# Performance work log

Measured on AMD Instinct MI355X. Metric: run time of the kernel, lower is better.

## Reference

```python
import jax, jax.numpy as jnp
import numpy as np

B, C, H, W = 2, 128, 64, 64


def setup_inputs() -> dict:
    key = jax.random.key(0)
    ks = jax.random.split(key, 16)
    s = 1.0 / np.sqrt(C)
    d = {
        "x": jax.random.normal(ks[0], (B, C, H, W), jnp.float32),
        "y": jax.random.normal(ks[1], (B, C, H, W), jnp.float32),
    }
    names = ["qr", "qi", "kr", "ki", "vr", "vi"]
    for i, n in enumerate(names):
        d["W" + n] = jax.random.normal(ks[2 + 2 * i], (C, C), jnp.float32) * s
        d["b" + n] = jax.random.normal(ks[3 + 2 * i], (C,), jnp.float32) * s
    return d


def _lin(t, Wt, bt):
    # t: [b, n, c]; torch Linear: t @ W^T + b
    return jnp.einsum("bnc,dc->bnd", t, Wt) + bt


def reference(x, y, Wqr, bqr, Wqi, bqi, Wkr, bkr, Wki, bki, Wvr, bvr, Wvi, bvi):
    b, c, h, w = x.shape
    xf = jnp.fft.fft2(x)  # over last two axes (h, w)
    yf = jnp.fft.fft2(y)
    # b c h w -> b (h w) c
    def flat(t):
        return t.transpose(0, 2, 3, 1).reshape(b, h * w, c)
    xr, xi = flat(xf.real), flat(xf.imag)
    yr, yi = flat(yf.real), flat(yf.imag)

    Qr = _lin(xr, Wqr, bqr) - _lin(xi, Wqi, bqi)
    Qi = _lin(xi, Wqr, bqr) + _lin(xr, Wqi, bqi)
    Kr = _lin(yr, Wkr, bkr) - _lin(yi, Wki, bki)
    Ki = _lin(yi, Wkr, bkr) + _lin(yr, Wki, bki)
    Vr = _lin(yr, Wvr, bvr) - _lin(yi, Wvi, bvi)
    Vi = _lin(yi, Wvr, bvr) + _lin(yr, Wvi, bvi)

    sr = jnp.einsum("bnc,bmc->bnm", Qr, Kr) - jnp.einsum("bnc,bmc->bnm", Qi, Ki)
    si = jnp.einsum("bnc,bmc->bnm", Qr, Ki) + jnp.einsum("bnc,bmc->bnm", Qi, Kr)
    scores = jnp.sqrt(sr * sr + si * si + 1e-8)
    attn = jax.nn.softmax(scores, axis=-1)

    out_r = jnp.einsum("bnm,bmc->bnc", attn, Vr)
    out_i = jnp.einsum("bnm,bmc->bnc", attn, Vi)
    out_c = jax.lax.complex(out_r, out_i)
    # b (h w) c -> b c h w
    out_c = out_c.reshape(b, h, w, c).transpose(0, 3, 1, 2)
    return jnp.fft.ifft2(out_c).real
```

## Files before the change

kernel.cpp:

```cpp
#include <hip/hip_runtime.h>
#include <math.h>


#define PI2 6.283185307179586f

typedef __attribute__((ext_vector_type(8))) short short8;
typedef __attribute__((ext_vector_type(4))) float f32x4;

#define MFMA16(A,B,C) __builtin_amdgcn_mfma_f32_16x16x32_bf16((A),(B),(C),0,0,0)

__device__ inline unsigned short f2bf(float x){
  union{float f; unsigned int u;} a; a.f = x;
  unsigned int r = (a.u + 0x7fffu + ((a.u>>16)&1u)) >> 16;
  return (unsigned short)r;
}
__device__ inline float bf2f(unsigned short h){
  union{unsigned int u; float f;} a; a.u = ((unsigned int)h)<<16; return a.f;
}
__device__ inline short8 neg8(short8 x){
  union{short8 v; unsigned int u[4];} a; a.v = x;
  a.u[0]^=0x80008000u; a.u[1]^=0x80008000u; a.u[2]^=0x80008000u; a.u[3]^=0x80008000u;
  return a.v;
}
__device__ inline void gload_lds16(const void* g, void* lds){
  __builtin_amdgcn_global_load_lds((const __attribute__((address_space(1))) unsigned int*)g,
                                   (__attribute__((address_space(3))) unsigned int*)lds,
                                   16, 0, 0);
}

__global__ __launch_bounds__(256) void dft2_fwd_kernel(
    const float* __restrict__ x, const float* __restrict__ y,
    float* __restrict__ xr, float* __restrict__ xi,
    float* __restrict__ yr, float* __restrict__ yi)
{
  __shared__ float Xs[4096];
  __shared__ float Tr[4096], Ti[4096];
  __shared__ float twc[64], tws[64];
  int blk = blockIdx.x;
  const float* src; float *outr, *outi;
  int plane;
  if (blk < 256) { src = x; outr = xr; outi = xi; plane = blk; }
  else           { src = y; outr = yr; outi = yi; plane = blk - 256; }
  int b = plane >> 7, c = plane & 127;
  int t = threadIdx.x;
  if (t < 64) {
    float ang = -PI2 * (float)t / 64.0f;
    twc[t] = cosf(ang); tws[t] = sinf(ang);
  }
  const float* p = src + ((size_t)plane << 12);
  for (int i = t; i < 4096; i += 256) Xs[i] = p[i];
  __syncthreads();
  for (int j = 0; j < 16; j++) {
    int o = t + 256 * j; int h = o >> 6, wp = o & 63;
    float ar = 0.f, ai = 0.f;
    for (int w = 0; w < 64; w++) {
      int k = (w * wp) & 63;
      float v = Xs[h * 64 + w];
      ar = fmaf(v, twc[k], ar);
      ai = fmaf(v, tws[k], ai);
    }
    Tr[h * 64 + wp] = ar; Ti[h * 64 + wp] = ai;
  }
  __syncthreads();
  size_t ob = ((size_t)b * 4096) * 128 + c;
  for (int j = 0; j < 16; j++) {
    int o = t + 256 * j; int hp = o >> 6, wp = o & 63;
    float ar = 0.f, ai = 0.f;
    for (int h = 0; h < 64; h++) {
      int k = (h * hp) & 63;
      float cr = twc[k], ci = tws[k];
      float tr = Tr[h * 64 + wp], ti = Ti[h * 64 + wp];
      ar += tr * cr - ti * ci;
      ai += tr * ci + ti * cr;
    }
    int n = (hp << 6) + wp;
    outr[ob + (size_t)n * 128] = ar;
    outi[ob + (size_t)n * 128] = ai;
  }
}

__global__ __launch_bounds__(256) void proj_kernel(
    const float* __restrict__ xr, const float* __restrict__ xi,
    const float* __restrict__ yr, const float* __restrict__ yi,
    const float* __restrict__ Wqr, const float* __restrict__ bqr,
    const float* __restrict__ Wqi, const float* __restrict__ bqi,
    const float* __restrict__ Wkr, const float* __restrict__ bkr,
    const float* __restrict__ Wki, const float* __restrict__ bki,
    const float* __restrict__ Wvr, const float* __restrict__ bvr,
    const float* __restrict__ Wvi, const float* __restrict__ bvi,
    unsigned short* __restrict__ FQ, unsigned short* __restrict__ FK,
    unsigned short* __restrict__ FV)
{
  __shared__ float Asr[64 * 33], Asi[64 * 33], Wsr[128 * 33], Wsi[128 * 33];
  int nt = blockIdx.x, lin = blockIdx.y, b = blockIdx.z;
  const float *ar, *ai, *Wr, *Wi, *br_, *bi_;
  unsigned short* F;
  if (lin == 0)      { ar = xr; ai = xi; Wr = Wqr; Wi = Wqi; br_ = bqr; bi_ = bqi; F = FQ; }
  else if (lin == 1) { ar = yr; ai = yi; Wr = Wkr; Wi = Wki; br_ = bkr; bi_ = bki; F = FK; }
  else               { ar = yr; ai = yi; Wr = Wvr; Wi = Wvi; br_ = bvr; bi_ = bvi; F = FV; }
  int t = threadIdx.x; int td = t & 15, tn = t >> 4;
  int n0 = nt * 64;
  size_t abase = (size_t)b * 4096 * 128 + (size_t)n0 * 128;
  const size_t PS = (size_t)2 * 4096 * 128;
  float accr[4][8] = {}, acci[4][8] = {};
  for (int kk = 0; kk < 4; kk++) {
    __syncthreads();
    for (int idx = t; idx < 64 * 32; idx += 256) {
      int r = idx >> 5, ccol = idx & 31;
      Asr[r * 33 + ccol] = ar[abase + (size_t)r * 128 + kk * 32 + ccol];
      Asi[r * 33 + ccol] = ai[abase + (size_t)r * 128 + kk * 32 + ccol];
    }
    for (int idx = t; idx < 128 * 32; idx += 256) {
      int r = idx >> 5, ccol = idx & 31;
      Wsr[r * 33 + ccol] = Wr[(size_t)r * 128 + kk * 32 + ccol];
      Wsi[r * 33 + ccol] = Wi[(size_t)r * 128 + kk * 32 + ccol];
    }
    __syncthreads();
    for (int k = 0; k < 32; k++) {
      float a_r[4], a_i[4], w_r[8], w_i[8];
      #pragma unroll
      for (int i = 0; i < 4; i++) {
        a_r[i] = Asr[(tn * 4 + i) * 33 + k];
        a_i[i] = Asi[(tn * 4 + i) * 33 + k];
      }
      #pragma unroll
      for (int jj = 0; jj < 8; jj++) {
        w_r[jj] = Wsr[(td + 16 * jj) * 33 + k];
        w_i[jj] = Wsi[(td + 16 * jj) * 33 + k];
      }
      #pragma unroll
      for (int i = 0; i < 4; i++)
        #pragma unroll
        for (int jj = 0; jj < 8; jj++) {
          accr[i][jj] += a_r[i] * w_r[jj] - a_i[i] * w_i[jj];
          acci[i][jj] += a_i[i] * w_r[jj] + a_r[i] * w_i[jj];
        }
    }
  }
  for (int jj = 0; jj < 8; jj++) {
    int d = td + 16 * jj;
    float brd = br_[d], bid = bi_[d];
    #pragma unroll
    for (int i = 0; i < 4; i++) {
      int n = n0 + tn * 4 + i;
      float cr = accr[i][jj] + (brd - bid);
      float ci = acci[i][jj] + (brd + bid);
      size_t base = ((size_t)b * 4096 + n) * 128 + d;
      if (lin <= 1) {
        unsigned short rh = f2bf(cr); unsigned short rl = f2bf(cr - bf2f(rh));
        unsigned short ih = f2bf(ci); unsigned short il = f2bf(ci - bf2f(ih));
        F[0 * PS + base] = rh;
        F[1 * PS + base] = rl;
        F[2 * PS + base] = ih;
        F[3 * PS + base] = il;
      } else {
        F[0 * PS + base] = f2bf(cr);
        F[1 * PS + base] = f2bf(ci);
      }
    }
  }
}

__global__ __launch_bounds__(256) void kpack_kernel(
    const unsigned short* __restrict__ F, unsigned short* __restrict__ Kpk)
{
  int blk = blockIdx.x;
  int b = blk >> 6, mt = blk & 63;
  int t = threadIdx.x;
  size_t obase = (size_t)blk * 4096;
  #pragma unroll
  for (int k = 0; k < 16; k++) {
    int idx = t + 256 * k;
    int l = idx & 63, s = (idx >> 6) & 3, tml = (idx >> 8) & 3, a = idx >> 10;
    int n = mt * 64 + tml * 16 + (l & 15);
    int c0 = 32 * s + 8 * (l >> 4);
    const short8 v = *(const short8*)(F + (((size_t)(a * 2 + b) * 4096 + n) * 128 + c0));
    *(short8*)(Kpk + (obase + idx) * 8) = v;
  }
}

__global__ __launch_bounds__(256) void vpack_kernel(
    const unsigned short* __restrict__ F, unsigned short* __restrict__ Vpk)
{
  __shared__ unsigned short Vs[2 * 32 * 128];
  int blk = blockIdx.x;
  int b = blk >> 7, sm = blk & 127;
  int t = threadIdx.x;
  const size_t PS = (size_t)2 * 4096 * 128;
  #pragma unroll
  for (int p = 0; p < 2; p++) {
    #pragma unroll
    for (int k = 0; k < 2; k++) {
      int idx8 = t + 256 * k;
      int nn = idx8 >> 4, d0 = (idx8 & 15) * 8;
      const short8 v = *(const short8*)(F + p * PS + ((size_t)(b * 4096 + sm * 32 + nn)) * 128 + d0);
      *(short8*)(Vs + (p * 32 + nn) * 128 + d0) = v;
    }
  }
  __syncthreads();
  size_t obase = (size_t)blk * 1024;
  #pragma unroll
  for (int k = 0; k < 4; k++) {
    int idx = t + 256 * k;
    int lv = idx & 63, tc = idx >> 6;
    int vh = tc >> 3;
    int d = (tc & 7) * 16 + (lv & 15);
    int nb = (lv >> 4) * 8;
    short8 v;
    #pragma unroll
    for (int j = 0; j < 8; j++)
      v[j] = (short)Vs[(vh * 32 + nb + j) * 128 + d];
    *(short8*)(Vpk + (obase + idx) * 8) = v;
  }
}

__global__ __launch_bounds__(256, 2) void attn_mfma_kernel(
    const unsigned short* __restrict__ FQ, const short* __restrict__ Kpk,
    const short* __restrict__ Vpk,
    float* __restrict__ Or_, float* __restrict__ Oi_)
{
  __shared__ __align__(16) short Klds[32768];
  __shared__ __align__(16) short Pfrag[16 * 72];
  __shared__ __align__(16) float rmax[16][4];

  const int bi = blockIdx.x;
  const int xg = bi & 7;
  const int b = xg >> 2;
  const int qt2 = (bi >> 3) * 4 + (xg & 3);
  const int t = threadIdx.x;
  const int ms = t >> 6, l = t & 63;
  const int g = l >> 4, c = l & 15;

  const size_t PS = (size_t)2 * 4096 * 128;
  short8 Qf[4][4];
  #pragma unroll
  for (int a = 0; a < 4; a++)
    #pragma unroll
    for (int s = 0; s < 4; s++)
      Qf[a][s] = *(const short8*)(FQ + (size_t)a * PS +
                 ((size_t)(b * 4096) + qt2 * 16 + c) * 128 + 32 * s + 8 * g);

  f32x4 O[4], Oe;
  #pragma unroll
  for (int nt = 0; nt < 4; nt++) O[nt] = (f32x4){0.f, 0.f, 0.f, 0.f};
  Oe = (f32x4){0.f, 0.f, 0.f, 0.f};
  float Mq = -3e38f, escPrev = 1.0f;
  bool upPrev = false;
  short8 Vreg[2][4];
  const short b1 = (short)0x3F80;
  const short8 ones = {b1, b1, b1, b1, b1, b1, b1, b1};
  const short8* Vp8 = (const short8*)Vpk;

  auto STAGE = [&](int tile) {
    const char* gsrc = (const char*)Kpk + ((size_t)(b * 64 + tile) << 16);
    #pragma unroll
    for (int i2 = 0; i2 < 16; i2++) {
      int ch = ms * 16 + i2;
      gload_lds16(gsrc + ch * 1024 + l * 16, (char*)Klds + ch * 1024);
    }
  };

  STAGE(0);
  asm volatile("s_waitcnt vmcnt(0)" ::: "memory");
  __builtin_amdgcn_s_barrier();
  __builtin_amdgcn_sched_barrier(0);

  f32x4 s0;
  for (int mt = 0; mt < 64; mt++) {
    if (mt > 0) {
      if (upPrev) {
        f32x4 esc4;
        #pragma unroll
        for (int r = 0; r < 4; r++) esc4[r] = __shfl(escPrev, 4 * g + r);
        #pragma unroll
        for (int r = 0; r < 4; r++) {
          #pragma unroll
          for (int nt = 0; nt < 4; nt++) O[nt][r] *= esc4[r];
          Oe[r] *= esc4[r];
        }
      }
      __builtin_amdgcn_s_setprio(1);
      #pragma unroll
      for (int ks = 0; ks < 2; ks++) {
        short8 Pa = *(const short8*)&Pfrag[c * 72 + 32 * ks + 8 * g];
        #pragma unroll
        for (int nt = 0; nt < 4; nt++)
          O[nt] = MFMA16(Pa, Vreg[ks][nt], O[nt]);
        Oe = MFMA16(Pa, ones, Oe);
      }
      __builtin_amdgcn_s_setprio(0);
    }
    const short8* kb8 = (const short8*)Klds;
    f32x4 sr0 = (f32x4){0,0,0,0}, sr1 = (f32x4){0,0,0,0};
    f32x4 si0 = (f32x4){0,0,0,0}, si1 = (f32x4){0,0,0,0};
    __builtin_amdgcn_s_setprio(1);
    #pragma unroll
    for (int s = 0; s < 4; s++) {
      short8 Arh = kb8[((0 * 4 + ms) * 4 + s) * 64 + l];
      short8 Arl = kb8[((1 * 4 + ms) * 4 + s) * 64 + l];
      short8 Aih = kb8[((2 * 4 + ms) * 4 + s) * 64 + l];
      short8 Ail = kb8[((3 * 4 + ms) * 4 + s) * 64 + l];
      short8 nqh = neg8(Qf[2][s]);
      short8 nql = neg8(Qf[3][s]);
      f32x4& sr = (s & 1) ? sr1 : sr0;
      f32x4& si = (s & 1) ? si1 : si0;
      sr = MFMA16(Arh, Qf[0][s], sr);
      si = MFMA16(Arh, Qf[2][s], si);
      sr = MFMA16(Arh, Qf[1][s], sr);
      si = MFMA16(Arh, Qf[3][s], si);
      sr = MFMA16(Arl, Qf[0][s], sr);
      si = MFMA16(Arl, Qf[2][s], si);
      sr = MFMA16(Aih, nqh, sr);
      si = MFMA16(Aih, Qf[0][s], si);
      sr = MFMA16(Aih, nql, sr);
      si = MFMA16(Aih, Qf[1][s], si);
      sr = MFMA16(Ail, nqh, sr);
      si = MFMA16(Ail, Qf[0][s], si);
    }
    __builtin_amdgcn_s_setprio(0);
    #pragma unroll
    for (int r = 0; r < 4; r++) {
      float a2 = sr0[r] + sr1[r], b2 = si0[r] + si1[r];
      s0[r] = sqrtf(a2 * a2 + b2 * b2 + 1e-8f);
    }
    float mloc = fmaxf(fmaxf(s0[0], s0[1]), fmaxf(s0[2], s0[3]));
    mloc = fmaxf(mloc, __shfl_xor(mloc, 16));
    mloc = fmaxf(mloc, __shfl_xor(mloc, 32));
    if (l < 16) rmax[l][ms] = mloc;
    asm volatile("s_waitcnt lgkmcnt(0)" ::: "memory");
    __builtin_amdgcn_s_barrier();
    __builtin_amdgcn_sched_barrier(0);
    if (mt + 1 < 64) STAGE(mt + 1);
    {
      f32x4 rm4 = *(const f32x4*)&rmax[c][0];
      float cand = fmaxf(fmaxf(rm4[0], rm4[1]), fmaxf(rm4[2], rm4[3]));
      bool up = !__all((int)(cand <= Mq + 8.0f));
      if (up) {
        float Mnew = fmaxf(Mq, cand);
        escPrev = __expf(Mq - Mnew);
        Mq = Mnew;
      }
      upPrev = up;
      f32x4 p;
      #pragma unroll
      for (int r = 0; r < 4; r++) p[r] = __expf(s0[r] - Mq);
      unsigned int* pw = (unsigned int*)&Pfrag[c * 72 + 16 * ms + 4 * g];
      pw[0] = (unsigned int)f2bf(p[0]) | ((unsigned int)f2bf(p[1]) << 16);
      pw[1] = (unsigned int)f2bf(p[2]) | ((unsigned int)f2bf(p[3]) << 16);
      #pragma unroll
      for (int ks = 0; ks < 2; ks++)
        #pragma unroll
        for (int nt = 0; nt < 4; nt++)
          Vreg[ks][nt] = Vp8[((size_t)((b * 128 + mt * 2 + ks) * 16 + ms * 4 + nt)) * 64 + l];
    }
    __builtin_amdgcn_sched_barrier(0);
    asm volatile("s_waitcnt vmcnt(8) lgkmcnt(0)" ::: "memory");
    __builtin_amdgcn_s_barrier();
    __builtin_amdgcn_sched_barrier(0);
  }
  {
    if (upPrev) {
      f32x4 esc4;
      #pragma unroll
      for (int r = 0; r < 4; r++) esc4[r] = __shfl(escPrev, 4 * g + r);
      #pragma unroll
      for (int r = 0; r < 4; r++) {
        #pragma unroll
        for (int nt = 0; nt < 4; nt++) O[nt][r] *= esc4[r];
        Oe[r] *= esc4[r];
      }
    }
    #pragma unroll
    for (int ks = 0; ks < 2; ks++) {
      short8 Pa = *(const short8*)&Pfrag[c * 72 + 32 * ks + 8 * g];
      #pragma unroll
      for (int nt = 0; nt < 4; nt++)
        O[nt] = MFMA16(Pa, Vreg[ks][nt], O[nt]);
      Oe = MFMA16(Pa, ones, Oe);
    }
  }
  const size_t base = (size_t)b * 4096 * 128;
  f32x4 inv;
  #pragma unroll
  for (int r = 0; r < 4; r++) inv[r] = 1.0f / Oe[r];
  #pragma unroll
  for (int nt = 0; nt < 4; nt++) {
    int cc = ms * 64 + nt * 16 + c;
    #pragma unroll
    for (int r = 0; r < 4; r++) {
      int row = qt2 * 16 + 4 * g + r;
      float v = O[nt][r] * inv[r];
      if (cc < 128) Or_[base + (size_t)row * 128 + cc] = v;
      else          Oi_[base + (size_t)row * 128 + cc - 128] = v;
    }
  }
}

__global__ __launch_bounds__(256) void idft2_kernel(
    const float* __restrict__ Or_, const float* __restrict__ Oi_,
    float* __restrict__ out)
{
  __shared__ float Ar[4096], Ai[4096], Tr[4096], Ti[4096];
  __shared__ float twc[64], tws[64];
  int plane = blockIdx.x; int b = plane >> 7, c = plane & 127;
  int t = threadIdx.x;
  if (t < 64) {
    float ang = PI2 * (float)t / 64.0f;
    twc[t] = cosf(ang); tws[t] = sinf(ang);
  }
  size_t ibase = (size_t)b * 4096 * 128 + c;
  for (int i = t; i < 4096; i += 256) {
    Ar[i] = Or_[ibase + (size_t)i * 128];
    Ai[i] = Oi_[ibase + (size_t)i * 128];
  }
  __syncthreads();
  for (int j = 0; j < 16; j++) {
    int o = t + 256 * j; int hp = o >> 6, w = o & 63;
    float tr = 0.f, ti = 0.f;
    for (int wp = 0; wp < 64; wp++) {
      int k = (wp * w) & 63;
      float cr = twc[k], ci = tws[k];
      float ar = Ar[hp * 64 + wp], ai = Ai[hp * 64 + wp];
      tr += ar * cr - ai * ci;
      ti += ai * cr + ar * ci;
    }
    Tr[hp * 64 + w] = tr; Ti[hp * 64 + w] = ti;
  }
  __syncthreads();
  size_t obase = ((size_t)plane) << 12;
  for (int j = 0; j < 16; j++) {
    int o = t + 256 * j; int h = o >> 6, w = o & 63;
    float acc = 0.f;
    for (int hp = 0; hp < 64; hp++) {
      int k = (hp * h) & 63;
      acc += Tr[hp * 64 + w] * twc[k] - Ti[hp * 64 + w] * tws[k];
    }
    out[obase + o] = acc * (1.0f / 4096.0f);
  }
}

extern "C" void kernel_launch(void* const* d_in, const int* in_sizes, int n_in,
                              void* d_out, int out_size, void* d_ws, size_t ws_size,
                              hipStream_t stream) {
  const float* x   = (const float*)d_in[0];
  const float* y   = (const float*)d_in[1];
  const float* Wqr = (const float*)d_in[2];  const float* bqr = (const float*)d_in[3];
  const float* Wqi = (const float*)d_in[4];  const float* bqi = (const float*)d_in[5];
  const float* Wkr = (const float*)d_in[6];  const float* bkr = (const float*)d_in[7];
  const float* Wki = (const float*)d_in[8];  const float* bki = (const float*)d_in[9];
  const float* Wvr = (const float*)d_in[10]; const float* bvr = (const float*)d_in[11];
  const float* Wvi = (const float*)d_in[12]; const float* bvi = (const float*)d_in[13];
  char* wsb = (char*)d_ws;
  if (ws_size < ((size_t)40 << 20)) return;
  unsigned short* FQ  = (unsigned short*)(wsb);
  unsigned short* FK  = (unsigned short*)(wsb + ((size_t)8  << 20));
  unsigned short* FV  = (unsigned short*)(wsb + ((size_t)16 << 20));
  float* xr = (float*)(wsb + ((size_t)20 << 20));
  float* xi = (float*)(wsb + ((size_t)24 << 20));
  float* yr = (float*)(wsb + ((size_t)28 << 20));
  float* yi = (float*)(wsb + ((size_t)32 << 20));
  unsigned short* Kpk = (unsigned short*)(wsb + ((size_t)28 << 20));
  unsigned short* Vpk = (unsigned short*)(wsb + ((size_t)36 << 20));
  float* Or_ = (float*)(wsb + ((size_t)20 << 20));
  float* Oi_ = (float*)(wsb + ((size_t)24 << 20));
  float* out = (float*)d_out;

  hipLaunchKernelGGL(dft2_fwd_kernel, dim3(512), dim3(256), 0, stream,
                     x, y, xr, xi, yr, yi);
  hipLaunchKernelGGL(proj_kernel, dim3(64, 3, 2), dim3(256), 0, stream,
                     xr, xi, yr, yi,
                     Wqr, bqr, Wqi, bqi, Wkr, bkr, Wki, bki, Wvr, bvr, Wvi, bvi,
                     FQ, FK, FV);
  hipLaunchKernelGGL(kpack_kernel, dim3(128), dim3(256), 0, stream, FK, Kpk);
  hipLaunchKernelGGL(vpack_kernel, dim3(256), dim3(256), 0, stream, FV, Vpk);
  hipLaunchKernelGGL(attn_mfma_kernel, dim3(512), dim3(256), 0, stream,
                     FQ, (const short*)Kpk, (const short*)Vpk, Or_, Oi_);
  hipLaunchKernelGGL(idft2_kernel, dim3(256), dim3(256), 0, stream,
                     Or_, Oi_, out);
}
```

Before: 405.0 us.

## Prefetch K tile into registers and issue next-tile staging earlier

Each wave now reads its whole K tile from LDS into registers at the top of the loop. It then immediately starts the global-to-LDS staging of the next tile instead of waiting until after the softmax-max barrier. The staging chunk mapping is reordered so each wave overwrites only the LDS chunks it has just read, which avoids any cross-wave hazard. V register loads are also moved earlier so they overlap the QK MFMAs. The aim is more overlap of global memory latency with compute, at the cost of about 64 extra VGPRs per lane for the K registers, which may reduce occupancy.

```diff
diff --git a/kernel.cpp b/kernel.cpp
--- a/kernel.cpp
+++ b/kernel.cpp
@@ -254,10 +254,12 @@
   auto STAGE = [&](int tile) {
     const char* gsrc = (const char*)Kpk + ((size_t)(b * 64 + tile) << 16);
     #pragma unroll
-    for (int i2 = 0; i2 < 16; i2++) {
-      int ch = ms * 16 + i2;
-      gload_lds16(gsrc + ch * 1024 + l * 16, (char*)Klds + ch * 1024);
-    }
+    for (int a = 0; a < 4; a++)
+      #pragma unroll
+      for (int s = 0; s < 4; s++) {
+        int ch = (a * 4 + ms) * 4 + s;
+        gload_lds16(gsrc + ch * 1024 + l * 16, (char*)Klds + ch * 1024);
+      }
   };
 
   STAGE(0);
@@ -265,8 +267,19 @@
   __builtin_amdgcn_s_barrier();
   __builtin_amdgcn_sched_barrier(0);
 
+  const short8* kb8 = (const short8*)Klds;
   f32x4 s0;
   for (int mt = 0; mt < 64; mt++) {
+    short8 Kreg[4][4];
+    #pragma unroll
+    for (int p = 0; p < 4; p++)
+      #pragma unroll
+      for (int s = 0; s < 4; s++)
+        Kreg[p][s] = kb8[((p * 4 + ms) * 4 + s) * 64 + l];
+    asm volatile("s_waitcnt lgkmcnt(0)" ::: "memory");
+    __builtin_amdgcn_sched_barrier(0);
+    if (mt + 1 < 64) STAGE(mt + 1);
+    __builtin_amdgcn_sched_barrier(0);
     if (mt > 0) {
       if (upPrev) {
         f32x4 esc4;
@@ -290,32 +303,33 @@
       }
       __builtin_amdgcn_s_setprio(0);
     }
-    const short8* kb8 = (const short8*)Klds;
+    #pragma unroll
+    for (int ks = 0; ks < 2; ks++)
+      #pragma unroll
+      for (int nt = 0; nt < 4; nt++)
+        Vreg[ks][nt] = Vp8[((size_t)((b * 128 + mt * 2 + ks) * 16 + ms * 4 + nt)) * 64 + l];
+    __builtin_amdgcn_sched_barrier(0);
     f32x4 sr0 = (f32x4){0,0,0,0}, sr1 = (f32x4){0,0,0,0};
     f32x4 si0 = (f32x4){0,0,0,0}, si1 = (f32x4){0,0,0,0};
     __builtin_amdgcn_s_setprio(1);
     #pragma unroll
     for (int s = 0; s < 4; s++) {
-      short8 Arh = kb8[((0 * 4 + ms) * 4 + s) * 64 + l];
-      short8 Arl = kb8[((1 * 4 + ms) * 4 + s) * 64 + l];
-      short8 Aih = kb8[((2 * 4 + ms) * 4 + s) * 64 + l];
-      short8 Ail = kb8[((3 * 4 + ms) * 4 + s) * 64 + l];
       short8 nqh = neg8(Qf[2][s]);
       short8 nql = neg8(Qf[3][s]);
       f32x4& sr = (s & 1) ? sr1 : sr0;
       f32x4& si = (s & 1) ? si1 : si0;
-      sr = MFMA16(Arh, Qf[0][s], sr);
-      si = MFMA16(Arh, Qf[2][s], si);
-      sr = MFMA16(Arh, Qf[1][s], sr);
-      si = MFMA16(Arh, Qf[3][s], si);
-      sr = MFMA16(Arl, Qf[0][s], sr);
-      si = MFMA16(Arl, Qf[2][s], si);
-      sr = MFMA16(Aih, nqh, sr);
-      si = MFMA16(Aih, Qf[0][s], si);
-      sr = MFMA16(Aih, nql, sr);
-      si = MFMA16(Aih, Qf[1][s], si);
-      sr = MFMA16(Ail, nqh, sr);
-      si = MFMA16(Ail, Qf[0][s], si);
+      sr = MFMA16(Kreg[0][s], Qf[0][s], sr);
+      si = MFMA16(Kreg[0][s], Qf[2][s], si);
+      sr = MFMA16(Kreg[0][s], Qf[1][s], sr);
+      si = MFMA16(Kreg[0][s], Qf[3][s], si);
+      sr = MFMA16(Kreg[1][s], Qf[0][s], sr);
+      si = MFMA16(Kreg[1][s], Qf[2][s], si);
+      sr = MFMA16(Kreg[2][s], nqh, sr);
+      si = MFMA16(Kreg[2][s], Qf[0][s], si);
+      sr = MFMA16(Kreg[2][s], nql, sr);
+      si = MFMA16(Kreg[2][s], Qf[1][s], si);
+      sr = MFMA16(Kreg[3][s], nqh, sr);
+      si = MFMA16(Kreg[3][s], Qf[0][s], si);
     }
     __builtin_amdgcn_s_setprio(0);
     #pragma unroll
@@ -330,7 +344,6 @@
     asm volatile("s_waitcnt lgkmcnt(0)" ::: "memory");
     __builtin_amdgcn_s_barrier();
     __builtin_amdgcn_sched_barrier(0);
-    if (mt + 1 < 64) STAGE(mt + 1);
     {
       f32x4 rm4 = *(const f32x4*)&rmax[c][0];
       float cand = fmaxf(fmaxf(rm4[0], rm4[1]), fmaxf(rm4[2], rm4[3]));
@@ -347,11 +360,6 @@
       unsigned int* pw = (unsigned int*)&Pfrag[c * 72 + 16 * ms + 4 * g];
       pw[0] = (unsigned int)f2bf(p[0]) | ((unsigned int)f2bf(p[1]) << 16);
       pw[1] = (unsigned int)f2bf(p[2]) | ((unsigned int)f2bf(p[3]) << 16);
-      #pragma unroll
-      for (int ks = 0; ks < 2; ks++)
-        #pragma unroll
-        for (int nt = 0; nt < 4; nt++)
-          Vreg[ks][nt] = Vp8[((size_t)((b * 128 + mt * 2 + ks) * 16 + ms * 4 + nt)) * 64 + l];
     }
     __builtin_amdgcn_sched_barrier(0);
     asm volatile("s_waitcnt vmcnt(8) lgkmcnt(0)" ::: "memory");
```

Measured after the change: 419.4 us. 1.04x slower.

## Software-pipeline attention loop to overlap QK of next tile with softmax/PV

Applied to the files above, without the earlier changes.

Restructures the attention main loop into a skewed pipeline: each iteration computes QK scores for tile mt while the softmax and PV for tile mt-1 (and PV for mt-2) run in the same iteration. Pfrag and rmax get double buffers indexed by parity, which removes one block barrier per iteration. The intent is to hide the barrier and softmax latency behind MFMA work. The cost is more live registers and a more complex prologue and epilogue. The STAGE load order is also reordered so chunks follow the (a,ms,s) indexing.

```diff
diff --git a/kernel.cpp b/kernel.cpp
--- a/kernel.cpp
+++ b/kernel.cpp
@@ -220,8 +220,8 @@
     float* __restrict__ Or_, float* __restrict__ Oi_)
 {
   __shared__ __align__(16) short Klds[32768];
-  __shared__ __align__(16) short Pfrag[16 * 72];
-  __shared__ __align__(16) float rmax[16][4];
+  __shared__ __align__(16) short Pfrag2[2][16 * 72];
+  __shared__ __align__(16) float rmax2[2][16][4];
 
   const int bi = blockIdx.x;
   const int xg = bi & 7;
@@ -250,47 +250,19 @@
   const short b1 = (short)0x3F80;
   const short8 ones = {b1, b1, b1, b1, b1, b1, b1, b1};
   const short8* Vp8 = (const short8*)Vpk;
+  const short8* kb8 = (const short8*)Klds;
 
   auto STAGE = [&](int tile) {
     const char* gsrc = (const char*)Kpk + ((size_t)(b * 64 + tile) << 16);
     #pragma unroll
-    for (int i2 = 0; i2 < 16; i2++) {
-      int ch = ms * 16 + i2;
-      gload_lds16(gsrc + ch * 1024 + l * 16, (char*)Klds + ch * 1024);
-    }
-  };
-
-  STAGE(0);
-  asm volatile("s_waitcnt vmcnt(0)" ::: "memory");
-  __builtin_amdgcn_s_barrier();
-  __builtin_amdgcn_sched_barrier(0);
-
-  f32x4 s0;
-  for (int mt = 0; mt < 64; mt++) {
-    if (mt > 0) {
-      if (upPrev) {
-        f32x4 esc4;
-        #pragma unroll
-        for (int r = 0; r < 4; r++) esc4[r] = __shfl(escPrev, 4 * g + r);
-        #pragma unroll
-        for (int r = 0; r < 4; r++) {
-          #pragma unroll
-          for (int nt = 0; nt < 4; nt++) O[nt][r] *= esc4[r];
-          Oe[r] *= esc4[r];
-        }
+    for (int a = 0; a < 4; a++)
+      #pragma unroll
+      for (int s = 0; s < 4; s++) {
+        int ch = (a * 4 + ms) * 4 + s;
+        gload_lds16(gsrc + ch * 1024 + l * 16, (char*)Klds + ch * 1024);
       }
-      __builtin_amdgcn_s_setprio(1);
-      #pragma unroll
-      for (int ks = 0; ks < 2; ks++) {
-        short8 Pa = *(const short8*)&Pfrag[c * 72 + 32 * ks + 8 * g];
-        #pragma unroll
-        for (int nt = 0; nt < 4; nt++)
-          O[nt] = MFMA16(Pa, Vreg[ks][nt], O[nt]);
-        Oe = MFMA16(Pa, ones, Oe);
-      }
-      __builtin_amdgcn_s_setprio(0);
-    }
-    const short8* kb8 = (const short8*)Klds;
+  };
+  auto QK = [&](f32x4& sout) {
     f32x4 sr0 = (f32x4){0,0,0,0}, sr1 = (f32x4){0,0,0,0};
     f32x4 si0 = (f32x4){0,0,0,0}, si1 = (f32x4){0,0,0,0};
     __builtin_amdgcn_s_setprio(1);
@@ -321,64 +293,111 @@
     #pragma unroll
     for (int r = 0; r < 4; r++) {
       float a2 = sr0[r] + sr1[r], b2 = si0[r] + si1[r];
-      s0[r] = sqrtf(a2 * a2 + b2 * b2 + 1e-8f);
-    }
+      sout[r] = sqrtf(a2 * a2 + b2 * b2 + 1e-8f);
+    }
+  };
+  auto WRMAX = [&](const f32x4& s0, int par) {
     float mloc = fmaxf(fmaxf(s0[0], s0[1]), fmaxf(s0[2], s0[3]));
     mloc = fmaxf(mloc, __shfl_xor(mloc, 16));
     mloc = fmaxf(mloc, __shfl_xor(mloc, 32));
-    if (l < 16) rmax[l][ms] = mloc;
+    if (l < 16) rmax2[par][l][ms] = mloc;
+  };
+  auto LOADV = [&](int mt) {
+    #pragma unroll
+    for (int ks = 0; ks < 2; ks++)
+      #pragma unroll
+      for (int nt = 0; nt < 4; nt++)
+        Vreg[ks][nt] = Vp8[((size_t)((b * 128 + mt * 2 + ks) * 16 + ms * 4 + nt)) * 64 + l];
+  };
+  auto RESCALE = [&]() {
+    f32x4 esc4;
+    #pragma unroll
+    for (int r = 0; r < 4; r++) esc4[r] = __shfl(escPrev, 4 * g + r);
+    #pragma unroll
+    for (int r = 0; r < 4; r++) {
+      #pragma unroll
+      for (int nt = 0; nt < 4; nt++) O[nt][r] *= esc4[r];
+      Oe[r] *= esc4[r];
+    }
+  };
+  auto PV = [&](int par) {
+    __builtin_amdgcn_s_setprio(1);
+    #pragma unroll
+    for (int ks = 0; ks < 2; ks++) {
+      short8 Pa = *(const short8*)&Pfrag2[par][c * 72 + 32 * ks + 8 * g];
+      #pragma unroll
+      for (int nt = 0; nt < 4; nt++)
+        O[nt] = MFMA16(Pa, Vreg[ks][nt], O[nt]);
+      Oe = MFMA16(Pa, ones, Oe);
+    }
+    __builtin_amdgcn_s_setprio(0);
+  };
+  auto SOFTMAX = [&](const f32x4& sPrev, int par) {
+    f32x4 rm4 = *(const f32x4*)&rmax2[par][c][0];
+    float cand = fmaxf(fmaxf(rm4[0], rm4[1]), fmaxf(rm4[2], rm4[3]));
+    bool up = !__all((int)(cand <= Mq + 8.0f));
+    if (up) {
+      float Mnew = fmaxf(Mq, cand);
+      escPrev = __expf(Mq - Mnew);
+      Mq = Mnew;
+    }
+    upPrev = up;
+    f32x4 p;
+    #pragma unroll
+    for (int r = 0; r < 4; r++) p[r] = __expf(sPrev[r] - Mq);
+    unsigned int* pw = (unsigned int*)&Pfrag2[par][c * 72 + 16 * ms + 4 * g];
+    pw[0] = (unsigned int)f2bf(p[0]) | ((unsigned int)f2bf(p[1]) << 16);
+    pw[1] = (unsigned int)f2bf(p[2]) | ((unsigned int)f2bf(p[3]) << 16);
+  };
+
+  STAGE(0);
+  asm volatile("s_waitcnt vmcnt(0)" ::: "memory");
+  __builtin_amdgcn_s_barrier();
+  __builtin_amdgcn_sched_barrier(0);
+
+  f32x4 s0prev, s0new;
+  QK(s0prev);
+  asm volatile("s_waitcnt lgkmcnt(0)" ::: "memory");
+  __builtin_amdgcn_sched_barrier(0);
+  STAGE(1);
+  __builtin_amdgcn_sched_barrier(0);
+  WRMAX(s0prev, 0);
+  asm volatile("s_waitcnt vmcnt(0) lgkmcnt(0)" ::: "memory");
+  __builtin_amdgcn_s_barrier();
+  __builtin_amdgcn_sched_barrier(0);
+
+  for (int mt = 1; mt < 64; mt++) {
+    const int p = mt & 1;
+    QK(s0new);
     asm volatile("s_waitcnt lgkmcnt(0)" ::: "memory");
-    __builtin_amdgcn_s_barrier();
     __builtin_amdgcn_sched_barrier(0);
     if (mt + 1 < 64) STAGE(mt + 1);
-    {
-      f32x4 rm4 = *(const f32x4*)&rmax[c][0];
-      float cand = fmaxf(fmaxf(rm4[0], rm4[1]), fmaxf(rm4[2], rm4[3]));
-      bool up = !__all((int)(cand <= Mq + 8.0f));
-      if (up) {
-        float Mnew = fmaxf(Mq, cand);
-        escPrev = __expf(Mq - Mnew);
-        Mq = Mnew;
-      }
-      upPrev = up;
-      f32x4 p;
-      #pragma unroll
-      for (int r = 0; r < 4; r++) p[r] = __expf(s0[r] - Mq);
-      unsigned int* pw = (unsigned int*)&Pfrag[c * 72 + 16 * ms + 4 * g];
-      pw[0] = (unsigned int)f2bf(p[0]) | ((unsigned int)f2bf(p[1]) << 16);
-      pw[1] = (unsigned int)f2bf(p[2]) | ((unsigned int)f2bf(p[3]) << 16);
-      #pragma unroll
-      for (int ks = 0; ks < 2; ks++)
-        #pragma unroll
-        for (int nt = 0; nt < 4; nt++)
-          Vreg[ks][nt] = Vp8[((size_t)((b * 128 + mt * 2 + ks) * 16 + ms * 4 + nt)) * 64 + l];
-    }
+    __builtin_amdgcn_sched_barrier(0);
+    if (mt >= 2) {
+      if (upPrev) RESCALE();
+      PV(p);
+    }
+    LOADV(mt - 1);
+    __builtin_amdgcn_sched_barrier(0);
+    SOFTMAX(s0prev, p ^ 1);
+    WRMAX(s0new, p);
+    s0prev = s0new;
     __builtin_amdgcn_sched_barrier(0);
     asm volatile("s_waitcnt vmcnt(8) lgkmcnt(0)" ::: "memory");
     __builtin_amdgcn_s_barrier();
     __builtin_amdgcn_sched_barrier(0);
   }
-  {
-    if (upPrev) {
-      f32x4 esc4;
-      #pragma unroll
-      for (int r = 0; r < 4; r++) esc4[r] = __shfl(escPrev, 4 * g + r);
-      #pragma unroll
-      for (int r = 0; r < 4; r++) {
-        #pragma unroll
-        for (int nt = 0; nt < 4; nt++) O[nt][r] *= esc4[r];
-        Oe[r] *= esc4[r];
-      }
-    }
-    #pragma unroll
-    for (int ks = 0; ks < 2; ks++) {
-      short8 Pa = *(const short8*)&Pfrag[c * 72 + 32 * ks + 8 * g];
-      #pragma unroll
-      for (int nt = 0; nt < 4; nt++)
-        O[nt] = MFMA16(Pa, Vreg[ks][nt], O[nt]);
-      Oe = MFMA16(Pa, ones, Oe);
-    }
-  }
+
+  if (upPrev) RESCALE();
+  PV(0);
+  LOADV(63);
+  SOFTMAX(s0prev, 1);
+  asm volatile("s_waitcnt lgkmcnt(0)" ::: "memory");
+  __builtin_amdgcn_s_barrier();
+  __builtin_amdgcn_sched_barrier(0);
+  if (upPrev) RESCALE();
+  PV(1);
+
   const size_t base = (size_t)b * 4096 * 128;
   f32x4 inv;
   #pragma unroll
```

Result: slower. 428.8 us (+5.9%).
